# Optimization experiments

Hardware: AMD Instinct MI355X
Metric: run time of the kernel (lower is better)

## Reference

```python
import jax, jax.numpy as jnp
import numpy as np
from jax import lax

WINDOW = 9
N_INT = 1000
WMSE_WEIGHTS = np.array([1.0, 2.0, 5.0, 10.0, 30.0], dtype=np.float32)
WMSE_THRESH = np.array([0.5, 2.0, 5.0, 10.0], dtype=np.float32)
LOSS_W = np.array([1e-4, 1.0], dtype=np.float32)


def setup_inputs() -> dict:
    key = jax.random.key(0)
    k1, k2 = jax.random.split(key)
    shape = (4, 1, 128, 128)
    return {
        "prediction": jax.random.normal(k1, shape, dtype=jnp.float32),
        "target": jax.random.normal(k2, shape, dtype=jnp.float32),
    }


def _box_mean(x, win):
    # Equivalent to the original shift-and-accumulate running mean: box sum over
    # in-bounds neighbors (edge-corrected mean). x: [B, 1, H, W].
    pad = win // 2
    k = jnp.ones((1, 1, win, win), x.dtype)
    num = lax.conv_general_dilated(x, k, (1, 1), [(pad, pad), (pad, pad)])
    ones = jnp.ones((1, 1) + x.shape[-2:], x.dtype)
    den = lax.conv_general_dilated(ones, k, (1, 1), [(pad, pad), (pad, pad)])
    return num / den


def _wmse(pred, tgt):
    # Threshold-weighted MSE: weight chosen by the largest threshold <= target.
    w = jnp.full_like(tgt, WMSE_WEIGHTS[0])
    for i in range(len(WMSE_THRESH)):
        w = jnp.where(tgt >= WMSE_THRESH[i], WMSE_WEIGHTS[i + 1], w)
    return jnp.mean(w * (pred - tgt) ** 2)


def _crps(pred, tgt, n):
    # Deterministic CRPS via numeric integration over n points spanning the
    # global data range: integral (H(x - pred) - H(x - tgt))^2 dx per pixel.
    lo = jnp.minimum(pred.min(), tgt.min())
    hi = jnp.maximum(pred.max(), tgt.max())
    x = jnp.linspace(lo, hi, n)
    dx = (hi - lo) / (n - 1)
    p = pred.reshape(-1)
    t = tgt.reshape(-1)
    Fp = x[:, None] >= p[None, :]  # [N_INT, n_pixels]
    Ft = x[:, None] >= t[None, :]
    sq = (Fp ^ Ft).astype(pred.dtype)  # (Fp - Ft)^2 for 0/1 indicators
    return jnp.mean(sq.sum(axis=0) * dx)


def reference(prediction, target):
    pred_dist = prediction - _box_mean(prediction, WINDOW)
    tgt_dist = target - _box_mean(target, WINDOW)
    wmse = _wmse(prediction, target)
    crps = _crps(pred_dist, tgt_dist, N_INT)
    return LOSS_W[0] * wmse + LOSS_W[1] * crps
```

## Files before the change

### kernel.cpp

```cpp
#include <hip/hip_runtime.h>


__global__ __launch_bounds__(256) void SPL_kA(const float* __restrict__ pred,
                                              const float* __restrict__ tgt,
                                              float* __restrict__ part,
                                              float2* __restrict__ dist) {
    __shared__ float sP[1280], sT[1280];
    __shared__ float vsP[256], vsT[256];
    __shared__ float red[12];

    int b = blockIdx.x;
    int t = threadIdx.x;
    int m  = b >> 6;
    int r2 = (b & 63) << 1;
    const float* p = pred + (m << 14);
    const float* q = tgt  + (m << 14);

#pragma unroll
    for (int s = 0; s < 5; ++s) {
        int k   = t + s * 256;
        int rr  = k >> 7;
        int cc  = k & 127;
        int grw = r2 - 4 + rr;
        bool ok = (unsigned)grw < 128u;
        sP[k] = ok ? p[(grw << 7) + cc] : 0.f;
        sT[k] = ok ? q[(grw << 7) + cc] : 0.f;
    }
    __syncthreads();

    int orow = t >> 7;
    int col  = t & 127;
    int row  = r2 + orow;

    float vp = 0.f, vt = 0.f;
    int vb = orow * 128 + col;
#pragma unroll
    for (int di = 0; di < 9; ++di) {
        vp += sP[vb + di * 128];
        vt += sT[vb + di * 128];
    }
    vsP[t] = vp; vsT[t] = vt;
    __syncthreads();

    float sp = 0.f, st = 0.f;
    int rbase = t & ~127;
#pragma unroll
    for (int dj = -4; dj <= 4; ++dj) {
        int jj = col + dj;
        if ((unsigned)jj < 128u) { sp += vsP[rbase + jj]; st += vsT[rbase + jj]; }
    }

    int   rc  = min(row, 4) + min(127 - row, 4) + 1;
    int   cn  = min(col, 4) + min(127 - col, 4) + 1;
    float den = (float)(rc * cn);
    float pv  = sP[(orow + 4) * 128 + col];
    float tv  = sT[(orow + 4) * 128 + col];
    float pd  = pv - sp / den;
    float td  = tv - st / den;

    dist[(b << 8) + t] = make_float2(pd, td);

    float w = 1.f;
    if (tv >= 0.5f) w = 2.f;
    if (tv >= 2.f)  w = 5.f;
    if (tv >= 5.f)  w = 10.f;
    if (tv >= 10.f) w = 30.f;
    float d  = pv - tv;
    float s  = w * d * d;
    float mn = fminf(pd, td);
    float mx = fmaxf(pd, td);

    for (int o = 32; o > 0; o >>= 1) {
        s  += __shfl_down(s, o, 64);
        mn  = fminf(mn, __shfl_down(mn, o, 64));
        mx  = fmaxf(mx, __shfl_down(mx, o, 64));
    }
    int lane = t & 63, wid = t >> 6;
    if (lane == 0) { red[wid] = s; red[4 + wid] = mn; red[8 + wid] = mx; }
    __syncthreads();
    if (t == 0) {
        part[b]       = red[0] + red[1] + red[2] + red[3];
        part[256 + b] = fminf(fminf(red[4], red[5]), fminf(red[6], red[7]));
        part[512 + b] = fmaxf(fmaxf(red[8], red[9]), fmaxf(red[10], red[11]));
    }
}

__global__ __launch_bounds__(1024) void SPL_kB(const float* __restrict__ part,
                                               const float2* __restrict__ dist,
                                               float* __restrict__ out) {
    __shared__ float rs[16], rmn[16], rmx[16];
    __shared__ int   rci[16];
    __shared__ float bc[3];

    int t = threadIdx.x;
    int lane = t & 63, wid = t >> 6;

    float s = 0.f, mn = 3.4e38f, mx = -3.4e38f;
    if (t < 256) { s = part[t]; mn = part[256 + t]; mx = part[512 + t]; }
    for (int o = 32; o > 0; o >>= 1) {
        s  += __shfl_down(s, o, 64);
        mn  = fminf(mn, __shfl_down(mn, o, 64));
        mx  = fmaxf(mx, __shfl_down(mx, o, 64));
    }
    if (lane == 0) { rs[wid] = s; rmn[wid] = mn; rmx[wid] = mx; }
    __syncthreads();
    if (t == 0) {
        float ss = 0.f, m1 = 3.4e38f, m2 = -3.4e38f;
        for (int i = 0; i < 16; ++i) {
            ss += rs[i]; m1 = fminf(m1, rmn[i]); m2 = fmaxf(m2, rmx[i]);
        }
        bc[0] = m1; bc[1] = m2; bc[2] = ss;
    }
    __syncthreads();

    float lo = bc[0], hi = bc[1];
    float dx = (hi - lo) / 999.0f;

    int cnt = 0;
#pragma unroll 4
    for (int it = 0; it < 64; ++it) {
        float2 d = dist[it * 1024 + t];
        float a  = fminf(d.x, d.y);
        float b2 = fmaxf(d.x, d.y);
        int ka = (int)ceilf((a - lo) / dx);
        int kb = (int)ceilf((b2 - lo) / dx);
        if (ka < 0) ka = 0;
        if (kb > 1000) kb = 1000;
        int c = kb - ka;
        if (c > 0) cnt += c;
    }
    for (int o = 32; o > 0; o >>= 1) cnt += __shfl_down(cnt, o, 64);
    if (lane == 0) rci[wid] = cnt;
    __syncthreads();
    if (t == 0) {
        long long tot = 0;
        for (int i = 0; i < 16; ++i) tot += rci[i];
        float  wmse = bc[2] * (1.0f / 65536.0f);
        double crps = (double)tot * (double)dx / 65536.0;
        out[0] = 1e-4f * wmse + (float)crps;
    }
}

extern "C" void kernel_launch(void* const* d_in, const int* in_sizes, int n_in,
                              void* d_out, int out_size, void* d_ws, size_t ws_size,
                              hipStream_t stream) {
    const float* pred = (const float*)d_in[0];
    const float* tgt  = (const float*)d_in[1];
    float*  part = (float*)d_ws;
    float2* dist = (float2*)(part + 768);
    float*  out  = (float*)d_out;

    SPL_kA<<<256, 256, 0, stream>>>(pred, tgt, part, dist);
    SPL_kB<<<1, 1024, 0, stream>>>(part, dist, out);
}
```

Measured before the change: 76.97 us.

## Fuse two kernels into one with a grid-wide spin barrier and last-block finalize

Merges the stencil/partial-reduction kernel and the single-block CRPS counting kernel into one kernel. A global atomic counter acts as a grid barrier so every block can read the global min/max, then each block counts its own pixels' CRPS bins in registers instead of writing and re-reading a distance buffer. The last block to finish does the final reduction. This drops a kernel launch and the serial single-block pass, but it adds a memset launch and relies on all 256 blocks being co-resident for the spin barrier.

Result: slower. 80.22 us (+4.2%).

```diff
diff --git a/kernel.cpp b/kernel.cpp
--- a/kernel.cpp
+++ b/kernel.cpp
@@ -1,13 +1,19 @@
 #include <hip/hip_runtime.h>
 
+#define GRID 256
+#define NTHR 256
 
-__global__ __launch_bounds__(256) void SPL_kA(const float* __restrict__ pred,
-                                              const float* __restrict__ tgt,
-                                              float* __restrict__ part,
-                                              float2* __restrict__ dist) {
+
+__global__ __launch_bounds__(256) void SPL_fused(const float* __restrict__ pred,
+                                                 const float* __restrict__ tgt,
+                                                 int* __restrict__ ctrl,
+                                                 float* __restrict__ part,
+                                                 float* __restrict__ out) {
     __shared__ float sP[1280], sT[1280];
     __shared__ float vsP[256], vsT[256];
     __shared__ float red[12];
+    __shared__ int   ired[4];
+    __shared__ int   amLast;
 
     int b = blockIdx.x;
     int t = threadIdx.x;
@@ -58,86 +64,81 @@
     float pd  = pv - sp / den;
     float td  = tv - st / den;
 
-    dist[(b << 8) + t] = make_float2(pd, td);
-
     float w = 1.f;
     if (tv >= 0.5f) w = 2.f;
     if (tv >= 2.f)  w = 5.f;
     if (tv >= 5.f)  w = 10.f;
     if (tv >= 10.f) w = 30.f;
     float d  = pv - tv;
-    float s  = w * d * d;
+    float s1 = w * d * d;
     float mn = fminf(pd, td);
     float mx = fmaxf(pd, td);
 
     for (int o = 32; o > 0; o >>= 1) {
-        s  += __shfl_down(s, o, 64);
+        s1 += __shfl_down(s1, o, 64);
         mn  = fminf(mn, __shfl_down(mn, o, 64));
         mx  = fmaxf(mx, __shfl_down(mx, o, 64));
     }
     int lane = t & 63, wid = t >> 6;
-    if (lane == 0) { red[wid] = s; red[4 + wid] = mn; red[8 + wid] = mx; }
+    if (lane == 0) { red[wid] = s1; red[4 + wid] = mn; red[8 + wid] = mx; }
     __syncthreads();
     if (t == 0) {
         part[b]       = red[0] + red[1] + red[2] + red[3];
         part[256 + b] = fminf(fminf(red[4], red[5]), fminf(red[6], red[7]));
         part[512 + b] = fmaxf(fmaxf(red[8], red[9]), fmaxf(red[10], red[11]));
     }
-}
 
-__global__ __launch_bounds__(1024) void SPL_kB(const float* __restrict__ part,
-                                               const float2* __restrict__ dist,
-                                               float* __restrict__ out) {
-    __shared__ float rs[16], rmn[16], rmx[16];
-    __shared__ int   rci[16];
-    __shared__ float bc[3];
-
-    int t = threadIdx.x;
-    int lane = t & 63, wid = t >> 6;
-
-    float s = 0.f, mn = 3.4e38f, mx = -3.4e38f;
-    if (t < 256) { s = part[t]; mn = part[256 + t]; mx = part[512 + t]; }
-    for (int o = 32; o > 0; o >>= 1) {
-        s  += __shfl_down(s, o, 64);
-        mn  = fminf(mn, __shfl_down(mn, o, 64));
-        mx  = fmaxf(mx, __shfl_down(mx, o, 64));
-    }
-    if (lane == 0) { rs[wid] = s; rmn[wid] = mn; rmx[wid] = mx; }
-    __syncthreads();
     if (t == 0) {
-        float ss = 0.f, m1 = 3.4e38f, m2 = -3.4e38f;
-        for (int i = 0; i < 16; ++i) {
-            ss += rs[i]; m1 = fminf(m1, rmn[i]); m2 = fmaxf(m2, rmx[i]);
-        }
-        bc[0] = m1; bc[1] = m2; bc[2] = ss;
+        __threadfence();
+        atomicAdd(&ctrl[0], 1);
+        while (__hip_atomic_load(&ctrl[0], __ATOMIC_ACQUIRE,
+                                 __HIP_MEMORY_SCOPE_AGENT) < GRID) { }
     }
     __syncthreads();
 
-    float lo = bc[0], hi = bc[1];
+    float mn2 = part[256 + t];
+    float mx2 = part[512 + t];
+    for (int o = 32; o > 0; o >>= 1) {
+        mn2 = fminf(mn2, __shfl_down(mn2, o, 64));
+        mx2 = fmaxf(mx2, __shfl_down(mx2, o, 64));
+    }
+    if (lane == 0) { red[wid] = mn2; red[4 + wid] = mx2; }
+    __syncthreads();
+    float lo = fminf(fminf(red[0], red[1]), fminf(red[2], red[3]));
+    float hi = fmaxf(fmaxf(red[4], red[5]), fmaxf(red[6], red[7]));
     float dx = (hi - lo) / 999.0f;
 
-    int cnt = 0;
-#pragma unroll 4
-    for (int it = 0; it < 64; ++it) {
-        float2 d = dist[it * 1024 + t];
-        float a  = fminf(d.x, d.y);
-        float b2 = fmaxf(d.x, d.y);
-        int ka = (int)ceilf((a - lo) / dx);
-        int kb = (int)ceilf((b2 - lo) / dx);
-        if (ka < 0) ka = 0;
-        if (kb > 1000) kb = 1000;
-        int c = kb - ka;
-        if (c > 0) cnt += c;
-    }
+    float a  = fminf(pd, td);
+    float b2 = fmaxf(pd, td);
+    int ka = (int)ceilf((a - lo) / dx);
+    int kb = (int)ceilf((b2 - lo) / dx);
+    ka = max(ka, 0);
+    kb = min(kb, 1000);
+    int cnt = max(kb - ka, 0);
     for (int o = 32; o > 0; o >>= 1) cnt += __shfl_down(cnt, o, 64);
-    if (lane == 0) rci[wid] = cnt;
+    if (lane == 0) ired[wid] = cnt;
     __syncthreads();
     if (t == 0) {
-        long long tot = 0;
-        for (int i = 0; i < 16; ++i) tot += rci[i];
-        float  wmse = bc[2] * (1.0f / 65536.0f);
-        double crps = (double)tot * (double)dx / 65536.0;
-        out[0] = 1e-4f * wmse + (float)crps;
+        int c = ired[0] + ired[1] + ired[2] + ired[3];
+        atomicAdd(&ctrl[2], c);
+        __threadfence();
+        int tk = atomicAdd(&ctrl[1], 1);
+        amLast = (tk == GRID - 1);
+    }
+    __syncthreads();
+
+    if (amLast) {
+        float ws_ = part[t];
+        for (int o = 32; o > 0; o >>= 1) ws_ += __shfl_down(ws_, o, 64);
+        if (lane == 0) red[wid] = ws_;
+        __syncthreads();
+        if (t == 0) {
+            float wtot = red[0] + red[1] + red[2] + red[3];
+            int   ctot = atomicAdd(&ctrl[2], 0);
+            float  wmse = wtot * (1.0f / 65536.0f);
+            double crps = (double)ctot * (double)dx / 65536.0;
+            out[0] = 1e-4f * wmse + (float)crps;
+        }
     }
 }
 
@@ -146,10 +147,10 @@
                               hipStream_t stream) {
     const float* pred = (const float*)d_in[0];
     const float* tgt  = (const float*)d_in[1];
-    float*  part = (float*)d_ws;
-    float2* dist = (float2*)(part + 768);
-    float*  out  = (float*)d_out;
+    int*   ctrl = (int*)d_ws;
+    float* part = (float*)d_ws + 4;
+    float* out  = (float*)d_out;
 
-    SPL_kA<<<256, 256, 0, stream>>>(pred, tgt, part, dist);
-    SPL_kB<<<1, 1024, 0, stream>>>(part, dist, out);
+    hipMemsetAsync(ctrl, 0, 16, stream);
+    SPL_fused<<<GRID, NTHR, 0, stream>>>(pred, tgt, ctrl, part, out);
 }
```
